# Kernel tuning notes

Measured on AMD Instinct MI355X. Metric: run time of the kernel, lower is better.

## Reference

```python
import jax, jax.numpy as jnp
import numpy as np

B, NQ, NK, D, H, DH = 4, 2048, 2048, 512, 8, 64  # inner_dim = H*DH = 512 = query_dim


def setup_inputs() -> dict:
    key = jax.random.key(0)
    ks = jax.random.split(key, 9)
    s = 0.02
    return {
        "init_query": jax.random.normal(ks[0], (B, NQ, D), dtype=jnp.float32),
        "embedding": jax.random.normal(ks[1], (B, NK, D), dtype=jnp.float32),
        "Wq": jax.random.normal(ks[2], (D, H * DH), dtype=jnp.float32) * s,
        "Wk": jax.random.normal(ks[3], (D, H * DH), dtype=jnp.float32) * s,
        "Wv": jax.random.normal(ks[4], (D, H * DH), dtype=jnp.float32) * s,
        "W0": jax.random.normal(ks[5], (H * DH, D), dtype=jnp.float32) * s,
        "b0": jnp.zeros((D,), dtype=jnp.float32),
        "W1": jax.random.normal(ks[6], (D, D), dtype=jnp.float32) * s,
        "b1": jnp.zeros((D,), dtype=jnp.float32),
    }


def reference(init_query, embedding, Wq, Wk, Wv, W0, b0, W1, b1):
    b, nq, _ = init_query.shape
    nk = embedding.shape[1]
    # project and split heads -> [b, h, n, dh]
    q = (init_query @ Wq).reshape(b, nq, H, DH).transpose(0, 2, 1, 3)
    k = (embedding @ Wk).reshape(b, nk, H, DH).transpose(0, 2, 1, 3)
    v = (embedding @ Wv).reshape(b, nk, H, DH).transpose(0, 2, 1, 3)
    # offset attention: alpha=1 (no 1/sqrt(d) scale)
    scores = jnp.einsum("bhqd,bhkd->bhqk", q, k)
    # softmax over the QUERY axis (torch dim=1 of [B*H, Nq, Nk]), then renormalize rows
    probs = jax.nn.softmax(scores, axis=2)
    probs = probs / (1e-12 + probs.sum(axis=-1, keepdims=True))
    out = jnp.einsum("bhqk,bhkd->bhqd", probs, v)
    out = out.transpose(0, 2, 1, 3).reshape(b, nq, H * DH)  # merge heads
    out = init_query - (out @ W0 + b0)  # offset residual
    out = out @ W1 + b1  # final projection (dropout p=0 -> identity)
    return out
```

## Files before the change

kernel.cpp:

```cpp
#include <hip/hip_runtime.h>
#include <math.h>

#define BATCH 4
#define NQ 2048
#define NKEY 2048
#define DMODEL 512
#define NH 8
#define DHEAD 64
#define BH (BATCH * NH)

typedef __attribute__((ext_vector_type(8))) short short8;
typedef __attribute__((ext_vector_type(4))) float f32x4;

#define MFMA16(a, b, c) __builtin_amdgcn_mfma_f32_16x16x32_bf16((a), (b), (c), 0, 0, 0)

static __device__ __forceinline__ unsigned short f2b(float f) {
    union { float f; unsigned u; } v; v.f = f;
    unsigned r = (v.u + 0x7fffu + ((v.u >> 16) & 1u)) >> 16;
    return (unsigned short)r;
}

__launch_bounds__(256) __global__
void cast_x(const float* __restrict__ a, const float* __restrict__ b,
            unsigned short* __restrict__ da, unsigned short* __restrict__ db) {
    const float* s = blockIdx.y ? b : a;
    unsigned short* d = blockIdx.y ? db : da;
    size_t i = ((size_t)blockIdx.x * 256 + threadIdx.x) * 4;
    float4 v = *(const float4*)(s + i);
    ushort4 o;
    o.x = f2b(v.x); o.y = f2b(v.y); o.z = f2b(v.z); o.w = f2b(v.w);
    *(ushort4*)(d + i) = o;
}

__launch_bounds__(256) __global__
void trans_w(const float* __restrict__ w0, const float* __restrict__ w1,
             const float* __restrict__ w2, const float* __restrict__ w3,
             const float* __restrict__ w4, unsigned short* __restrict__ dst) {
    const float* src = (blockIdx.z == 0) ? w0 : (blockIdx.z == 1) ? w1 :
                       (blockIdx.z == 2) ? w2 : (blockIdx.z == 3) ? w3 : w4;
    unsigned short* out = dst + (size_t)blockIdx.z * DMODEL * DMODEL;
    __shared__ float t[32][33];
    const int tx = threadIdx.x & 31, ty = threadIdx.x >> 5;
    const int k0 = blockIdx.x * 32, n0 = blockIdx.y * 32;
    #pragma unroll
    for (int j = 0; j < 4; ++j)
        t[ty + j * 8][tx] = src[(size_t)(k0 + ty + j * 8) * DMODEL + n0 + tx];
    __syncthreads();
    #pragma unroll
    for (int j = 0; j < 4; ++j)
        out[(size_t)(n0 + ty + j * 8) * DMODEL + k0 + tx] = f2b(t[tx][ty + j * 8]);
}

__device__ __forceinline__
void gemm_core(const unsigned short* __restrict__ A0,
               const unsigned short* __restrict__ B0,
               int K, int tid, unsigned short* Al, unsigned short* Bl,
               f32x4 acc[2][4]) {
    const int w = tid >> 6, lane = tid & 63;
    const int l16 = lane & 15, q4 = lane >> 4;
    char* AlB = (char*)Al;
    char* BlB = (char*)Bl;
    const int srow = tid >> 3;
    const int scolb = (tid & 7) * 16;
    const int skoff = (tid & 7) * 8;

    f32x4 z = {0.f, 0.f, 0.f, 0.f};
    #pragma unroll
    for (int i = 0; i < 2; ++i)
        #pragma unroll
        for (int t = 0; t < 4; ++t) acc[i][t] = z;

    short8 ast[4], bst[2];
    #pragma unroll
    for (int c = 0; c < 4; ++c)
        ast[c] = *(const short8*)(A0 + (size_t)(c * 32 + srow) * K + skoff);
    #pragma unroll
    for (int c = 0; c < 2; ++c)
        bst[c] = *(const short8*)(B0 + (size_t)(c * 32 + srow) * K + skoff);

    for (int k0 = 0; k0 < K; k0 += 64) {
        __syncthreads();
        #pragma unroll
        for (int c = 0; c < 4; ++c) {
            const int row = c * 32 + srow;
            *(short8*)(AlB + row * 128 + (scolb ^ ((row & 7) << 4))) = ast[c];
        }
        #pragma unroll
        for (int c = 0; c < 2; ++c) {
            const int row = c * 32 + srow;
            *(short8*)(BlB + row * 128 + (scolb ^ ((row & 7) << 4))) = bst[c];
        }
        if (k0 + 64 < K) {
            #pragma unroll
            for (int c = 0; c < 4; ++c)
                ast[c] = *(const short8*)(A0 + (size_t)(c * 32 + srow) * K + k0 + 64 + skoff);
            #pragma unroll
            for (int c = 0; c < 2; ++c)
                bst[c] = *(const short8*)(B0 + (size_t)(c * 32 + srow) * K + k0 + 64 + skoff);
        }
        __syncthreads();

        #pragma unroll
        for (int kk = 0; kk < 2; ++kk) {
            const int kb = kk * 64;
            const int rswA0 = ((w * 32 + l16) & 7) << 4;
            short8 a0 = *(const short8*)(AlB + (w * 32 + l16) * 128 + ((kb + q4 * 16) ^ rswA0));
            short8 a1 = *(const short8*)(AlB + (w * 32 + 16 + l16) * 128 + ((kb + q4 * 16) ^ rswA0));
            short8 bfr[4];
            #pragma unroll
            for (int t = 0; t < 4; ++t) {
                const int row = t * 16 + l16;
                bfr[t] = *(const short8*)(BlB + row * 128 + ((kb + q4 * 16) ^ ((row & 7) << 4)));
            }
            #pragma unroll
            for (int t = 0; t < 4; ++t) {
                acc[0][t] = MFMA16(a0, bfr[t], acc[0][t]);
                acc[1][t] = MFMA16(a1, bfr[t], acc[1][t]);
            }
        }
    }
}

__launch_bounds__(256) __global__
void gemm_qkv(const unsigned short* __restrict__ Xq,
              const unsigned short* __restrict__ Xe,
              const unsigned short* __restrict__ Wt,
              unsigned short* __restrict__ Qh,
              unsigned short* __restrict__ Kh,
              unsigned short* __restrict__ Vtb) {
    __shared__ unsigned short Al[128 * 64];
    __shared__ unsigned short Bl[64 * 64];
    const int tid = threadIdx.x;
    const int zsel = blockIdx.z;
    const int K = DMODEL;
    const unsigned short* A = (zsel == 0) ? Xq : Xe;
    const unsigned short* B0 = Wt + (size_t)zsel * DMODEL * DMODEL + (size_t)(blockIdx.y * 64) * K;
    const unsigned short* A0 = A + (size_t)(blockIdx.x * 128) * K;

    f32x4 acc[2][4];
    gemm_core(A0, B0, K, tid, Al, Bl, acc);

    const int w = tid >> 6, lane = tid & 63;
    const int l16 = lane & 15, q4 = lane >> 4;
    const int mBase = blockIdx.x * 128 + w * 32;
    const int n0 = blockIdx.y * 64;

    if (zsel < 2) {
        unsigned short* out = (zsel == 0) ? Qh : Kh;
        #pragma unroll
        for (int i = 0; i < 2; ++i)
            #pragma unroll
            for (int t = 0; t < 4; ++t)
                #pragma unroll
                for (int r = 0; r < 4; ++r) {
                    const int m = mBase + i * 16 + q4 * 4 + r;
                    const int n = n0 + t * 16 + l16;
                    out[(((size_t)(m >> 11) * NH + (n >> 6)) * NQ + (m & 2047)) * DHEAD + (n & 63)] = f2b(acc[i][t][r]);
                }
    } else {
        #pragma unroll
        for (int i = 0; i < 2; ++i)
            #pragma unroll
            for (int t = 0; t < 4; ++t) {
                const int m0 = mBase + i * 16 + q4 * 4;
                const int n = n0 + t * 16 + l16;
                ushort4 p;
                p.x = f2b(acc[i][t][0]); p.y = f2b(acc[i][t][1]);
                p.z = f2b(acc[i][t][2]); p.w = f2b(acc[i][t][3]);
                *(ushort4*)(Vtb + (((size_t)(m0 >> 11) * NH + (n >> 6)) * DHEAD + (n & 63)) * NKEY + (m0 & 2047)) = p;
            }
    }
}

template <int MODE>
__launch_bounds__(256) __global__
void gemm_bf16(const unsigned short* __restrict__ A,
               const unsigned short* __restrict__ Bt,
               void* __restrict__ Cout, const float* __restrict__ bias,
               const float* __restrict__ resid, int M, int N, int K) {
    __shared__ unsigned short Al[128 * 64];
    __shared__ unsigned short Bl[64 * 64];
    const int tid = threadIdx.x;
    const unsigned short* A0 = A + (size_t)(blockIdx.x * 128) * K;
    const unsigned short* B0 = Bt + (size_t)(blockIdx.y * 64) * K;

    f32x4 acc[2][4];
    gemm_core(A0, B0, K, tid, Al, Bl, acc);

    const int w = tid >> 6, lane = tid & 63;
    const int l16 = lane & 15, q4 = lane >> 4;
    const int mBase = blockIdx.x * 128 + w * 32;
    const int n0 = blockIdx.y * 64;

    #pragma unroll
    for (int i = 0; i < 2; ++i)
        #pragma unroll
        for (int t = 0; t < 4; ++t)
            #pragma unroll
            for (int r = 0; r < 4; ++r) {
                const int m = mBase + i * 16 + q4 * 4 + r;
                const int n = n0 + t * 16 + l16;
                float v = acc[i][t][r];
                if (MODE == 2) {
                    ((unsigned short*)Cout)[(size_t)m * N + n] = f2b(resid[(size_t)m * N + n] - (v + bias[n]));
                } else {
                    ((float*)Cout)[(size_t)m * N + n] = v + bias[n];
                }
            }
}

__launch_bounds__(512) __global__
void attn_pass1(const unsigned short* __restrict__ Qh,
                const unsigned short* __restrict__ Kh,
                float* __restrict__ colSrcp) {
    __shared__ unsigned short Qt[2][64 * 64];
    const int tid = threadIdx.x;
    const int w = tid >> 6, lane = tid & 63;
    const int l16 = lane & 15, q4 = lane >> 4;
    const int bh = blockIdx.y;
    const int kcol0 = blockIdx.x * 128 + w * 16;

    short8 bk0, bk1;
    {
        const unsigned short* Krow = Kh + ((size_t)bh * NKEY + kcol0 + l16) * DHEAD;
        bk0 = *(const short8*)(Krow + q4 * 8);
        bk1 = *(const short8*)(Krow + 32 + q4 * 8);
    }
    const unsigned short* Qb = Qh + (size_t)bh * NQ * DHEAD;
    const int srow = tid >> 3;
    const int skoff = (tid & 7) * 8;
    const int ssw = ((tid & 7) * 16) ^ ((srow & 7) << 4);
    const int rsw = (l16 & 7) << 4;

    f32x4 z = {0.f, 0.f, 0.f, 0.f};
    float csum = 0.f;

    short8 qst = *(const short8*)(Qb + (size_t)srow * DHEAD + skoff);
    *(short8*)((char*)Qt[0] + srow * 128 + ssw) = qst;
    qst = *(const short8*)(Qb + (size_t)(64 + srow) * DHEAD + skoff);
    __syncthreads();

    for (int it = 0; it < 32; ++it) {
        const int q0 = it * 64;
        char* QtB = (char*)Qt[it & 1];
        char* QtN = (char*)Qt[(it & 1) ^ 1];

        if (it < 31) {
            *(short8*)(QtN + srow * 128 + ssw) = qst;
            if (it < 30)
                qst = *(const short8*)(Qb + (size_t)(q0 + 128 + srow) * DHEAD + skoff);
        }

        #pragma unroll
        for (int qi = 0; qi < 4; ++qi) {
            const int row = qi * 16 + l16;
            short8 a0 = *(const short8*)(QtB + row * 128 + ((q4 * 16) ^ rsw));
            short8 a1 = *(const short8*)(QtB + row * 128 + ((64 + q4 * 16) ^ rsw));
            f32x4 s = MFMA16(a0, bk0, z);
            s = MFMA16(a1, bk1, s);
            csum += __expf(s[0]) + __expf(s[1]) + __expf(s[2]) + __expf(s[3]);
        }
        __syncthreads();
    }
    csum += __shfl_xor(csum, 16, 64);
    csum += __shfl_xor(csum, 32, 64);
    if (q4 == 0)
        colSrcp[(size_t)bh * NKEY + kcol0 + l16] = 1.0f / csum;
}

__launch_bounds__(512) __global__
void attn_pass2(const unsigned short* __restrict__ Qh,
                const unsigned short* __restrict__ Kh,
                const unsigned short* __restrict__ Vt,
                const float* __restrict__ colSrcp,
                unsigned short* __restrict__ attnb) {
    __shared__ unsigned short Kt[2][64 * 64];
    __shared__ unsigned short Vtile[2][64 * 64];
    __shared__ unsigned short Elds[8][2][16][40];
    const int tid = threadIdx.x;
    const int w = tid >> 6, lane = tid & 63;
    const int l16 = lane & 15, q4 = lane >> 4;
    const int bh = blockIdx.y;
    const int b = bh >> 3, h = bh & 7;
    const int q0w = blockIdx.x * 128 + w * 16;

    short8 aq0, aq1;
    {
        const unsigned short* Qrow = Qh + ((size_t)bh * NQ + q0w + l16) * DHEAD;
        aq0 = *(const short8*)(Qrow + q4 * 8);
        aq1 = *(const short8*)(Qrow + 32 + q4 * 8);
    }
    const unsigned short* Kb = Kh + (size_t)bh * NKEY * DHEAD;
    const unsigned short* Vb = Vt + (size_t)bh * DHEAD * NKEY;
    const float* cs = colSrcp + (size_t)bh * NKEY;
    unsigned short* Ew = &Elds[w][0][0][0];

    const int srow = tid >> 3;
    const int skoff = (tid & 7) * 8;
    const int ssw = ((tid & 7) * 16) ^ ((srow & 7) << 4);
    const int rsw = (l16 & 7) << 4;

    f32x4 z = {0.f, 0.f, 0.f, 0.f};
    f32x4 o[4];
    #pragma unroll
    for (int t = 0; t < 4; ++t) o[t] = z;
    float rq[4] = {};

    short8 kst = *(const short8*)(Kb + (size_t)srow * DHEAD + skoff);
    short8 vst = *(const short8*)(Vb + (size_t)srow * NKEY + skoff);
    *(short8*)((char*)Kt[0] + srow * 128 + ssw) = kst;
    *(short8*)((char*)Vtile[0] + srow * 128 + ssw) = vst;
    kst = *(const short8*)(Kb + (size_t)(64 + srow) * DHEAD + skoff);
    vst = *(const short8*)(Vb + (size_t)srow * NKEY + 64 + skoff);
    __syncthreads();

    for (int it = 0; it < 32; ++it) {
        const int k0 = it * 64;
        char* KtB = (char*)Kt[it & 1];
        char* VtB = (char*)Vtile[it & 1];
        char* KtN = (char*)Kt[(it & 1) ^ 1];
        char* VtN = (char*)Vtile[(it & 1) ^ 1];

        float rcp[2][2];
        #pragma unroll
        for (int sub = 0; sub < 2; ++sub)
            #pragma unroll
            for (int j = 0; j < 2; ++j)
                rcp[sub][j] = cs[k0 + sub * 32 + j * 16 + l16];

        if (it < 31) {
            *(short8*)(KtN + srow * 128 + ssw) = kst;
            *(short8*)(VtN + srow * 128 + ssw) = vst;
            if (it < 30) {
                kst = *(const short8*)(Kb + (size_t)(k0 + 128 + srow) * DHEAD + skoff);
                vst = *(const short8*)(Vb + (size_t)srow * NKEY + (k0 + 128) + skoff);
            }
        }

        #pragma unroll
        for (int sub = 0; sub < 2; ++sub) {
            short8 bk[2][2];
            #pragma unroll
            for (int j = 0; j < 2; ++j) {
                const int row = sub * 32 + j * 16 + l16;
                bk[j][0] = *(const short8*)(KtB + row * 128 + ((q4 * 16) ^ rsw));
                bk[j][1] = *(const short8*)(KtB + row * 128 + ((64 + q4 * 16) ^ rsw));
            }
            short8 bv[4];
            #pragma unroll
            for (int t = 0; t < 4; ++t) {
                const int row = t * 16 + l16;
                bv[t] = *(const short8*)(VtB + row * 128 + ((sub * 64 + q4 * 16) ^ rsw));
            }
            unsigned short* Eb = Ew + sub * (16 * 40);
            #pragma unroll
            for (int j = 0; j < 2; ++j) {
                f32x4 s = MFMA16(aq0, bk[j][0], z);
                s = MFMA16(aq1, bk[j][1], s);
                #pragma unroll
                for (int r = 0; r < 4; ++r) {
                    float e = __expf(s[r]) * rcp[sub][j];
                    rq[r] += e;
                    Eb[(q4 * 4 + r) * 40 + j * 16 + l16] = f2b(e);
                }
            }
            short8 ea = *(const short8*)(Eb + l16 * 40 + q4 * 8);
            #pragma unroll
            for (int t = 0; t < 4; ++t)
                o[t] = MFMA16(ea, bv[t], o[t]);
        }
        __syncthreads();
    }

    #pragma unroll
    for (int r = 0; r < 4; ++r) {
        float v = rq[r];
        v += __shfl_xor(v, 1, 64);
        v += __shfl_xor(v, 2, 64);
        v += __shfl_xor(v, 4, 64);
        v += __shfl_xor(v, 8, 64);
        rq[r] = 1.0f / (1e-12f + v);
    }
    #pragma unroll
    for (int t = 0; t < 4; ++t)
        #pragma unroll
        for (int r = 0; r < 4; ++r) {
            const int q = q0w + q4 * 4 + r;
            attnb[((size_t)b * NQ + q) * DMODEL + h * DHEAD + t * 16 + l16] =
                f2b(o[t][r] * rq[r]);
        }
}

extern "C" void kernel_launch(void* const* d_in, const int* in_sizes, int n_in,
                              void* d_out, int out_size, void* d_ws, size_t ws_size,
                              hipStream_t stream) {
    const float* init_query = (const float*)d_in[0];
    const float* embedding  = (const float*)d_in[1];
    const float* Wq = (const float*)d_in[2];
    const float* Wk = (const float*)d_in[3];
    const float* Wv = (const float*)d_in[4];
    const float* W0 = (const float*)d_in[5];
    const float* b0 = (const float*)d_in[6];
    const float* W1 = (const float*)d_in[7];
    const float* b1 = (const float*)d_in[8];
    float* out = (float*)d_out;

    const size_t ACT = (size_t)BATCH * NQ * DMODEL;
    const size_t WEL = (size_t)DMODEL * DMODEL;

    unsigned short* Xq   = (unsigned short*)d_ws;
    unsigned short* Xe   = Xq + ACT;
    unsigned short* Wt   = Xe + ACT;
    unsigned short* Qh   = Wt + 5 * WEL;
    unsigned short* Kh   = Qh + ACT;
    unsigned short* Vtb  = Kh + ACT;
    unsigned short* attnb= Vtb + ACT;
    unsigned short* ybuf = attnb + ACT;
    float* colSrcp = (float*)(ybuf + ACT);

    unsigned short* W0t = Wt + 3 * WEL;
    unsigned short* W1t = Wt + 4 * WEL;

    const int M = BATCH * NQ;
    dim3 blk(256);
    dim3 blk512(512);
    dim3 gGemm(M / 128, DMODEL / 64);

    cast_x<<<dim3(ACT / 1024, 2), blk, 0, stream>>>(init_query, embedding, Xq, Xe);
    trans_w<<<dim3(16, 16, 5), blk, 0, stream>>>(Wq, Wk, Wv, W0, W1, Wt);

    gemm_qkv<<<dim3(M / 128, DMODEL / 64, 3), blk, 0, stream>>>(Xq, Xe, Wt, Qh, Kh, Vtb);

    attn_pass1<<<dim3(NKEY / 128, BH), blk512, 0, stream>>>(Qh, Kh, colSrcp);
    attn_pass2<<<dim3(NQ / 128, BH), blk512, 0, stream>>>(Qh, Kh, Vtb, colSrcp, attnb);

    gemm_bf16<2><<<gGemm, blk, 0, stream>>>(attnb, W0t, ybuf, b0, init_query, M, DMODEL, DMODEL);
    gemm_bf16<3><<<gGemm, blk, 0, stream>>>(ybuf, W1t, out, b1, nullptr, M, DMODEL, DMODEL);
}
```

Before: 227.1 us.

## Fold column softmax reciprocals into V and compute row sums via extra MFMA

Adds a scale_v kernel that multiplies the transposed V by the per-key column-softmax reciprocal, so pass2 no longer scales each exp by rcp. The row normaliser is now an extra MFMA against a bf16 reciprocal vector instead of scalar sums and shuffles. The QK^T MFMA operands are swapped so exp results pack directly into LDS as uint2, and s_setprio hints are placed around the MFMA blocks. This trades an extra elementwise pass over V and bf16 rounding of the scales for less VALU work in the inner loop.

```diff
diff --git a/kernel.cpp b/kernel.cpp
--- a/kernel.cpp
+++ b/kernel.cpp
@@ -18,6 +18,10 @@
     union { float f; unsigned u; } v; v.f = f;
     unsigned r = (v.u + 0x7fffu + ((v.u >> 16) & 1u)) >> 16;
     return (unsigned short)r;
+}
+static __device__ __forceinline__ float b2f(unsigned short u) {
+    union { unsigned u; float f; } v; v.u = ((unsigned)u) << 16;
+    return v.f;
 }
 
 __launch_bounds__(256) __global__
@@ -212,7 +216,8 @@
 __launch_bounds__(512) __global__
 void attn_pass1(const unsigned short* __restrict__ Qh,
                 const unsigned short* __restrict__ Kh,
-                float* __restrict__ colSrcp) {
+                float* __restrict__ colSrcp,
+                unsigned short* __restrict__ cbuf) {
     __shared__ unsigned short Qt[2][64 * 64];
     const int tid = threadIdx.x;
     const int w = tid >> 6, lane = tid & 63;
@@ -256,27 +261,53 @@
             const int row = qi * 16 + l16;
             short8 a0 = *(const short8*)(QtB + row * 128 + ((q4 * 16) ^ rsw));
             short8 a1 = *(const short8*)(QtB + row * 128 + ((64 + q4 * 16) ^ rsw));
+            __builtin_amdgcn_s_setprio(1);
             f32x4 s = MFMA16(a0, bk0, z);
             s = MFMA16(a1, bk1, s);
+            __builtin_amdgcn_s_setprio(0);
             csum += __expf(s[0]) + __expf(s[1]) + __expf(s[2]) + __expf(s[3]);
         }
         __syncthreads();
     }
     csum += __shfl_xor(csum, 16, 64);
     csum += __shfl_xor(csum, 32, 64);
-    if (q4 == 0)
-        colSrcp[(size_t)bh * NKEY + kcol0 + l16] = 1.0f / csum;
+    if (q4 == 0) {
+        const float c = 1.0f / csum;
+        colSrcp[(size_t)bh * NKEY + kcol0 + l16] = c;
+        cbuf[(size_t)bh * NKEY + kcol0 + l16] = f2b(c);
+    }
+}
+
+__launch_bounds__(256) __global__
+void scale_v(unsigned short* __restrict__ Vtb, const float* __restrict__ colSrcp) {
+    const size_t t8 = ((size_t)blockIdx.x * 256 + threadIdx.x) * 8;
+    const int k = (int)(t8 & (NKEY - 1));
+    const int bh = (int)(t8 >> 17);
+    const float* cs = colSrcp + ((size_t)bh << 11) + k;
+    short8 v = *(const short8*)(Vtb + t8);
+    float4 c0 = *(const float4*)cs;
+    float4 c1 = *(const float4*)(cs + 4);
+    short8 o;
+    o[0] = (short)f2b(b2f((unsigned short)v[0]) * c0.x);
+    o[1] = (short)f2b(b2f((unsigned short)v[1]) * c0.y);
+    o[2] = (short)f2b(b2f((unsigned short)v[2]) * c0.z);
+    o[3] = (short)f2b(b2f((unsigned short)v[3]) * c0.w);
+    o[4] = (short)f2b(b2f((unsigned short)v[4]) * c1.x);
+    o[5] = (short)f2b(b2f((unsigned short)v[5]) * c1.y);
+    o[6] = (short)f2b(b2f((unsigned short)v[6]) * c1.z);
+    o[7] = (short)f2b(b2f((unsigned short)v[7]) * c1.w);
+    *(short8*)(Vtb + t8) = o;
 }
 
 __launch_bounds__(512) __global__
 void attn_pass2(const unsigned short* __restrict__ Qh,
                 const unsigned short* __restrict__ Kh,
                 const unsigned short* __restrict__ Vt,
-                const float* __restrict__ colSrcp,
+                const unsigned short* __restrict__ cb,
                 unsigned short* __restrict__ attnb) {
     __shared__ unsigned short Kt[2][64 * 64];
     __shared__ unsigned short Vtile[2][64 * 64];
-    __shared__ unsigned short Elds[8][2][16][40];
+    __shared__ unsigned short Elds[8][16][40];
     const int tid = threadIdx.x;
     const int w = tid >> 6, lane = tid & 63;
     const int l16 = lane & 15, q4 = lane >> 4;
@@ -292,8 +323,8 @@
     }
     const unsigned short* Kb = Kh + (size_t)bh * NKEY * DHEAD;
     const unsigned short* Vb = Vt + (size_t)bh * DHEAD * NKEY;
-    const float* cs = colSrcp + (size_t)bh * NKEY;
-    unsigned short* Ew = &Elds[w][0][0][0];
+    const unsigned short* cbb = cb + (size_t)bh * NKEY;
+    char* Ew = (char*)&Elds[w][0][0];
 
     const int srow = tid >> 3;
     const int skoff = (tid & 7) * 8;
@@ -304,7 +335,7 @@
     f32x4 o[4];
     #pragma unroll
     for (int t = 0; t < 4; ++t) o[t] = z;
-    float rq[4] = {};
+    f32x4 o5 = z;
 
     short8 kst = *(const short8*)(Kb + (size_t)srow * DHEAD + skoff);
     short8 vst = *(const short8*)(Vb + (size_t)srow * NKEY + skoff);
@@ -321,13 +352,6 @@
         char* KtN = (char*)Kt[(it & 1) ^ 1];
         char* VtN = (char*)Vtile[(it & 1) ^ 1];
 
-        float rcp[2][2];
-        #pragma unroll
-        for (int sub = 0; sub < 2; ++sub)
-            #pragma unroll
-            for (int j = 0; j < 2; ++j)
-                rcp[sub][j] = cs[k0 + sub * 32 + j * 16 + l16];
-
         if (it < 31) {
             *(short8*)(KtN + srow * 128 + ssw) = kst;
             *(short8*)(VtN + srow * 128 + ssw) = vst;
@@ -339,12 +363,13 @@
 
         #pragma unroll
         for (int sub = 0; sub < 2; ++sub) {
+            const int kb = k0 + sub * 32;
             short8 bk[2][2];
             #pragma unroll
-            for (int j = 0; j < 2; ++j) {
-                const int row = sub * 32 + j * 16 + l16;
-                bk[j][0] = *(const short8*)(KtB + row * 128 + ((q4 * 16) ^ rsw));
-                bk[j][1] = *(const short8*)(KtB + row * 128 + ((64 + q4 * 16) ^ rsw));
+            for (int jt = 0; jt < 2; ++jt) {
+                const int row = sub * 32 + jt * 16 + l16;
+                bk[jt][0] = *(const short8*)(KtB + row * 128 + ((q4 * 16) ^ rsw));
+                bk[jt][1] = *(const short8*)(KtB + row * 128 + ((64 + q4 * 16) ^ rsw));
             }
             short8 bv[4];
             #pragma unroll
@@ -352,42 +377,40 @@
                 const int row = t * 16 + l16;
                 bv[t] = *(const short8*)(VtB + row * 128 + ((sub * 64 + q4 * 16) ^ rsw));
             }
-            unsigned short* Eb = Ew + sub * (16 * 40);
-            #pragma unroll
-            for (int j = 0; j < 2; ++j) {
-                f32x4 s = MFMA16(aq0, bk[j][0], z);
-                s = MFMA16(aq1, bk[j][1], s);
-                #pragma unroll
-                for (int r = 0; r < 4; ++r) {
-                    float e = __expf(s[r]) * rcp[sub][j];
-                    rq[r] += e;
-                    Eb[(q4 * 4 + r) * 40 + j * 16 + l16] = f2b(e);
-                }
-            }
-            short8 ea = *(const short8*)(Eb + l16 * 40 + q4 * 8);
+            short8 bv5 = *(const short8*)(cbb + kb + q4 * 8);
+
+            #pragma unroll
+            for (int jt = 0; jt < 2; ++jt) {
+                __builtin_amdgcn_s_setprio(1);
+                f32x4 st = MFMA16(bk[jt][0], aq0, z);
+                st = MFMA16(bk[jt][1], aq1, st);
+                __builtin_amdgcn_s_setprio(0);
+                uint2 p;
+                p.x = (unsigned)f2b(__expf(st[0])) | ((unsigned)f2b(__expf(st[1])) << 16);
+                p.y = (unsigned)f2b(__expf(st[2])) | ((unsigned)f2b(__expf(st[3])) << 16);
+                *(uint2*)(Ew + l16 * 80 + jt * 32 + q4 * 8) = p;
+            }
+            short8 ea = *(const short8*)(Ew + l16 * 80 + q4 * 16);
+            __builtin_amdgcn_s_setprio(1);
             #pragma unroll
             for (int t = 0; t < 4; ++t)
                 o[t] = MFMA16(ea, bv[t], o[t]);
+            o5 = MFMA16(ea, bv5, o5);
+            __builtin_amdgcn_s_setprio(0);
         }
         __syncthreads();
     }
 
-    #pragma unroll
-    for (int r = 0; r < 4; ++r) {
-        float v = rq[r];
-        v += __shfl_xor(v, 1, 64);
-        v += __shfl_xor(v, 2, 64);
-        v += __shfl_xor(v, 4, 64);
-        v += __shfl_xor(v, 8, 64);
-        rq[r] = 1.0f / (1e-12f + v);
-    }
+    float rr[4];
+    #pragma unroll
+    for (int r = 0; r < 4; ++r) rr[r] = 1.0f / (1e-12f + o5[r]);
     #pragma unroll
     for (int t = 0; t < 4; ++t)
         #pragma unroll
         for (int r = 0; r < 4; ++r) {
             const int q = q0w + q4 * 4 + r;
             attnb[((size_t)b * NQ + q) * DMODEL + h * DHEAD + t * 16 + l16] =
-                f2b(o[t][r] * rq[r]);
+                f2b(o[t][r] * rr[r]);
         }
 }
 
@@ -418,6 +441,8 @@
     unsigned short* ybuf = attnb + ACT;
     float* colSrcp = (float*)(ybuf + ACT);
 
+    unsigned short* cbuf = ybuf;
+
     unsigned short* W0t = Wt + 3 * WEL;
     unsigned short* W1t = Wt + 4 * WEL;
 
@@ -431,8 +456,9 @@
 
     gemm_qkv<<<dim3(M / 128, DMODEL / 64, 3), blk, 0, stream>>>(Xq, Xe, Wt, Qh, Kh, Vtb);
 
-    attn_pass1<<<dim3(NKEY / 128, BH), blk512, 0, stream>>>(Qh, Kh, colSrcp);
-    attn_pass2<<<dim3(NQ / 128, BH), blk512, 0, stream>>>(Qh, Kh, Vtb, colSrcp, attnb);
+    attn_pass1<<<dim3(NKEY / 128, BH), blk512, 0, stream>>>(Qh, Kh, colSrcp, cbuf);
+    scale_v<<<dim3(ACT / 2048), blk, 0, stream>>>(Vtb, colSrcp);
+    attn_pass2<<<dim3(NQ / 128, BH), blk512, 0, stream>>>(Qh, Kh, Vtb, cbuf, attnb);
 
     gemm_bf16<2><<<gGemm, blk, 0, stream>>>(attnb, W0t, ybuf, b0, init_query, M, DMODEL, DMODEL);
     gemm_bf16<3><<<gGemm, blk, 0, stream>>>(ybuf, W1t, out, b1, nullptr, M, DMODEL, DMODEL);
```

Result: no change. 226.1 us (-0.5%).
